# Kernel optimization log

Hardware: AMD Instinct MI355X
Metric: run time of the kernel (lower is better)

The kernel has to match this reference:

```python
import jax, jax.numpy as jnp
import numpy as np

NUM_HEADS = 12
HEAD_DIM = 64
HIDDEN = NUM_HEADS * HEAD_DIM  # 768
B, L = 4, 512

def setup_inputs() -> dict:
    key = jax.random.key(0)
    ks = jax.random.split(key, 8)
    s = 0.02
    return {
        "hidden_states": jax.random.normal(ks[0], (B, L, HIDDEN), jnp.float32),
        "relation_embedding_k": jax.random.normal(ks[1], (B, L, L, HEAD_DIM), jnp.float32),
        "relation_embedding_v": jax.random.normal(ks[2], (B, L, L, HEAD_DIM), jnp.float32),
        "Wq": jax.random.normal(ks[3], (HIDDEN, HIDDEN), jnp.float32) * s,
        "bq": jnp.zeros((HIDDEN,), jnp.float32),
        "Wk": jax.random.normal(ks[4], (HIDDEN, HIDDEN), jnp.float32) * s,
        "bk": jnp.zeros((HIDDEN,), jnp.float32),
        "Wv": jax.random.normal(ks[5], (HIDDEN, HIDDEN), jnp.float32) * s,
        "bv": jnp.zeros((HIDDEN,), jnp.float32),
    }

def _heads(x):
    # [B, L, HIDDEN] -> [B, H, L, D]
    b, l, _ = x.shape
    return x.reshape(b, l, NUM_HEADS, HEAD_DIM).transpose(0, 2, 1, 3)

def reference(hidden_states, relation_embedding_k, relation_embedding_v,
              Wq, bq, Wk, bk, Wv, bv):
    q = _heads(hidden_states @ Wq + bq)  # [B,H,L,D]
    k = _heads(hidden_states @ Wk + bk)
    v = _heads(hidden_states @ Wv + bv)

    # content scores + relation key scores (shared across heads)
    scores = jnp.einsum('bhld,bhmd->bhlm', q, k)
    scores = scores + jnp.einsum('bhld,blrd->bhlr', q, relation_embedding_k)
    scores = scores / np.sqrt(HEAD_DIM).astype(np.float32)

    probs = jax.nn.softmax(scores, axis=-1)  # [B,H,L,L]

    ctx = jnp.einsum('bhlm,bhmd->bhld', probs, v)
    ctx = ctx + jnp.einsum('bhlr,brld->bhld', probs, relation_embedding_v)

    # [B,H,L,D] -> [B,L,HIDDEN]
    b, h, l, d = ctx.shape
    return ctx.transpose(0, 2, 1, 3).reshape(b, l, h * d)
```

## Files before the change

kernel.cpp:

```cpp
#include <hip/hip_runtime.h>
#include <stdint.h>


typedef __attribute__((ext_vector_type(8))) short bf16x8;
typedef __attribute__((ext_vector_type(4))) float f32x4;
typedef __attribute__((ext_vector_type(4))) unsigned int u32x4;
typedef __attribute__((ext_vector_type(2))) unsigned int u32x2;

__device__ __forceinline__ unsigned short f2bf(float f) {
  union { float f; unsigned int u; } v; v.f = f;
  unsigned int r = v.u + 0x7fffu + ((v.u >> 16) & 1u);
  return (unsigned short)(r >> 16);
}
__device__ __forceinline__ float bf2f(unsigned short s) {
  union { unsigned int u; float f; } v; v.u = ((unsigned int)s) << 16;
  return v.f;
}
__device__ __forceinline__ void lds_barrier() {
  asm volatile("s_waitcnt lgkmcnt(0)\ns_barrier" ::: "memory");
}

__global__ void k_cvt_hidden(const float* __restrict__ x, unsigned short* __restrict__ y) {
  int i = blockIdx.x * 256 + threadIdx.x;
  float4 v = reinterpret_cast<const float4*>(x)[i];
  ushort4 o;
  o.x = f2bf(v.x); o.y = f2bf(v.y); o.z = f2bf(v.z); o.w = f2bf(v.w);
  reinterpret_cast<ushort4*>(y)[i] = o;
}

__global__ void k_transp_w(const float* __restrict__ Wq, const float* __restrict__ Wk,
                           const float* __restrict__ Wv, unsigned short* __restrict__ wt) {
  __shared__ float t[64][65];
  const int kt = blockIdx.x, nt = blockIdx.y, wsel = blockIdx.z;
  const float* W = wsel == 0 ? Wq : (wsel == 1 ? Wk : Wv);
  const int lx = threadIdx.x & 63, ly = threadIdx.x >> 6;
  for (int i = 0; i < 64; i += 4)
    t[ly + i][lx] = W[(size_t)(kt * 64 + ly + i) * 768 + nt * 64 + lx];
  __syncthreads();
  for (int i = 0; i < 64; i += 4) {
    int r = ly + i;
    wt[((size_t)wsel * 768 + nt * 64 + r) * 768 + kt * 64 + lx] = f2bf(t[lx][r]);
  }
}

__global__ __launch_bounds__(256) void k_qkv_gemm(
    const unsigned short* __restrict__ A, const unsigned short* __restrict__ Bt,
    const float* __restrict__ bq, const float* __restrict__ bk, const float* __restrict__ bv,
    unsigned short* __restrict__ qbf, unsigned short* __restrict__ kbf,
    unsigned short* __restrict__ vbt) {
  __shared__ __align__(16) unsigned short lA[64 * 64];
  __shared__ __align__(16) unsigned short lB[64 * 64];
  const int tid = threadIdx.x, lane = tid & 63, w = tid >> 6;
  const int m0 = blockIdx.x * 64, n0 = blockIdx.y * 64;
  const int wm = (w >> 1) * 32, wn = (w & 1) * 32;
  f32x4 acc[2][2] = {};

  for (int kt = 0; kt < 12; ++kt) {
    __syncthreads();
#pragma unroll
    for (int i = 0; i < 2; ++i) {
      int e16 = i * 256 + tid;
      int row = e16 >> 3;
      int kb = (e16 & 7) * 16;
      int dst = row * 128 + (kb ^ ((row & 7) << 4));
      u32x4 va = *(const u32x4*)((const char*)A + (size_t)(m0 + row) * 1536 + kt * 128 + kb);
      *(u32x4*)((char*)lA + dst) = va;
      u32x4 vb = *(const u32x4*)((const char*)Bt + (size_t)(n0 + row) * 1536 + kt * 128 + kb);
      *(u32x4*)((char*)lB + dst) = vb;
    }
    __syncthreads();
#pragma unroll
    for (int ks = 0; ks < 2; ++ks) {
      bf16x8 fa[2], fb[2];
      const int kbyte = (ks * 32 + (lane >> 4) * 8) * 2;
#pragma unroll
      for (int mi = 0; mi < 2; ++mi) {
        int row = wm + mi * 16 + (lane & 15);
        fa[mi] = *(const bf16x8*)((const char*)lA + row * 128 + (kbyte ^ ((row & 7) << 4)));
      }
#pragma unroll
      for (int ni = 0; ni < 2; ++ni) {
        int row = wn + ni * 16 + (lane & 15);
        fb[ni] = *(const bf16x8*)((const char*)lB + row * 128 + (kbyte ^ ((row & 7) << 4)));
      }
#pragma unroll
      for (int mi = 0; mi < 2; ++mi)
#pragma unroll
        for (int ni = 0; ni < 2; ++ni)
          acc[mi][ni] = __builtin_amdgcn_mfma_f32_16x16x32_bf16(fa[mi], fb[ni], acc[mi][ni], 0, 0, 0);
    }
  }
#pragma unroll
  for (int mi = 0; mi < 2; ++mi)
#pragma unroll
    for (int ni = 0; ni < 2; ++ni) {
      int gn = n0 + wn + ni * 16 + (lane & 15);
      float bias = (gn < 768) ? bq[gn] : (gn < 1536 ? bk[gn - 768] : bv[gn - 1536]);
#pragma unroll
      for (int r = 0; r < 4; ++r) {
        int gm = m0 + wm + mi * 16 + ((lane >> 4) << 2) + r;
        float val = acc[mi][ni][r] + bias;
        int b = gm >> 9, l = gm & 511;
        int d = gn & 63;
        if (gn < 768) {
          int h = gn >> 6;
          qbf[(((size_t)(b * 12 + h)) * 512 + l) * 64 + d] = f2bf(val);
        } else if (gn < 1536) {
          int h = (gn - 768) >> 6;
          kbf[(((size_t)(b * 12 + h)) * 512 + l) * 64 + d] = f2bf(val);
        } else {
          int h = (gn - 1536) >> 6;
          vbt[(((size_t)(b * 12 + h)) * 64 + d) * 512 + l] = f2bf(val);
        }
      }
    }
}

__global__ __launch_bounds__(256) void k_scores(
    const unsigned short* __restrict__ qbf, const unsigned short* __restrict__ kbf,
    float* __restrict__ S) {
  __shared__ __align__(16) unsigned short lQ[64 * 64];
  __shared__ __align__(16) unsigned short lK[64 * 64];
  const int tid = threadIdx.x, lane = tid & 63, w = tid >> 6;
  const int mt = blockIdx.x, lt = blockIdx.y, bh = blockIdx.z;
  const int wm = (w >> 1) * 32, wn = (w & 1) * 32;
  f32x4 acc[2][2] = {};
#pragma unroll
  for (int i = 0; i < 2; ++i) {
    int e16 = i * 256 + tid;
    int row = e16 >> 3;
    int kb = (e16 & 7) * 16;
    int dst = row * 128 + (kb ^ ((row & 7) << 4));
    u32x4 vq = *(const u32x4*)((const char*)qbf + ((size_t)bh * 512 + lt * 64 + row) * 128 + kb);
    *(u32x4*)((char*)lQ + dst) = vq;
    u32x4 vk = *(const u32x4*)((const char*)kbf + ((size_t)bh * 512 + mt * 64 + row) * 128 + kb);
    *(u32x4*)((char*)lK + dst) = vk;
  }
  __syncthreads();
#pragma unroll
  for (int ks = 0; ks < 2; ++ks) {
    bf16x8 fa[2], fb[2];
    const int kbyte = (ks * 32 + (lane >> 4) * 8) * 2;
#pragma unroll
    for (int mi = 0; mi < 2; ++mi) {
      int row = wm + mi * 16 + (lane & 15);
      fa[mi] = *(const bf16x8*)((const char*)lQ + row * 128 + (kbyte ^ ((row & 7) << 4)));
    }
#pragma unroll
    for (int ni = 0; ni < 2; ++ni) {
      int row = wn + ni * 16 + (lane & 15);
      fb[ni] = *(const bf16x8*)((const char*)lK + row * 128 + (kbyte ^ ((row & 7) << 4)));
    }
#pragma unroll
    for (int mi = 0; mi < 2; ++mi)
#pragma unroll
      for (int ni = 0; ni < 2; ++ni)
        acc[mi][ni] = __builtin_amdgcn_mfma_f32_16x16x32_bf16(fa[mi], fb[ni], acc[mi][ni], 0, 0, 0);
  }
#pragma unroll
  for (int mi = 0; mi < 2; ++mi)
#pragma unroll
    for (int ni = 0; ni < 2; ++ni) {
      int gm = mt * 64 + wn + ni * 16 + (lane & 15);
#pragma unroll
      for (int r = 0; r < 4; ++r) {
        int gl = lt * 64 + wm + mi * 16 + ((lane >> 4) << 2) + r;
        S[(size_t)bh * 262144 + (size_t)gl * 512 + gm] = acc[mi][ni][r];
      }
    }
}

__global__ __launch_bounds__(256, 3) void k_rel(
    const unsigned short* __restrict__ qbf,
    const float* __restrict__ relk,
    const float* __restrict__ relv,
    const float* __restrict__ S,
    unsigned short* __restrict__ pbf,
    float* __restrict__ crel) {
  __shared__ __align__(16) char X[32768];
  __shared__ __align__(16) unsigned short ps[16 * 512];
  const int tid = threadIdx.x, lane = tid & 63, w = tid >> 6;
  const int bl = blockIdx.x, b = bl >> 9, l = bl & 511;
  const int lm = lane & 15, lg = lane >> 4;
  const int rr = tid >> 4, xc = tid & 15;

  {
    u32x4 zz = {0u, 0u, 0u, 0u};
    *(u32x4*)((char*)ps + 12288 + tid * 16) = zz;
  }

  const int hq = lm < 12 ? lm : 11;
  const char* qrow = (const char*)qbf + (((size_t)b * 12 + hq) * 512 + l) * 128;
  const bf16x8 qa0 = *(const bf16x8*)(qrow + lg * 16);
  const bf16x8 qa1 = *(const bf16x8*)(qrow + 64 + lg * 16);

  const char* rkbase = (const char*)relk + (size_t)bl * 131072;
  const char* rvbase = (const char*)relv + (size_t)b * 67108864 + (size_t)l * 256;

  f32x4 stg[2][8];
  f32x4 accA[4][2];
#pragma unroll
  for (int t = 0; t < 4; ++t) {
    accA[t][0] = {0.f, 0.f, 0.f, 0.f};
    accA[t][1] = {0.f, 0.f, 0.f, 0.f};
  }

#pragma unroll
  for (int i = 0; i < 8; ++i)
    stg[0][i] = *(const f32x4*)(rkbase + (size_t)(i * 16 + rr) * 256 + xc * 16);

#pragma unroll
  for (int t = 0; t < 4; ++t) {
    if (t < 3) {
#pragma unroll
      for (int i = 0; i < 8; ++i)
        stg[(t + 1) & 1][i] =
            *(const f32x4*)(rkbase + (size_t)((t + 1) * 128 + i * 16 + rr) * 256 + xc * 16);
    }
    char* buf = X + (t & 1) * 16384;
#pragma unroll
    for (int i = 0; i < 8; ++i) {
      const int rl = i * 16 + rr;
      f32x4 v = stg[t & 1][i];
      u32x2 pk;
      pk.x = (unsigned)f2bf(v[0]) | ((unsigned)f2bf(v[1]) << 16);
      pk.y = (unsigned)f2bf(v[2]) | ((unsigned)f2bf(v[3]) << 16);
      *(u32x2*)(buf + rl * 128 + ((xc * 8) ^ ((rl & 7) << 4))) = pk;
    }
    lds_barrier();
#pragma unroll
    for (int p = 0; p < 2; ++p) {
      const int rrow = (w * 2 + p) * 16 + lm;
      const char* base = buf + rrow * 128;
      bf16x8 fb0 = *(const bf16x8*)(base + ((lg * 16) ^ ((rrow & 7) << 4)));
      bf16x8 fb1 = *(const bf16x8*)(base + ((64 + lg * 16) ^ ((rrow & 7) << 4)));
      accA[t][p] = __builtin_amdgcn_mfma_f32_16x16x32_bf16(qa0, fb0, accA[t][p], 0, 0, 0);
      accA[t][p] = __builtin_amdgcn_mfma_f32_16x16x32_bf16(qa1, fb1, accA[t][p], 0, 0, 0);
    }
  }

  float sreg[3][8];
#pragma unroll
  for (int hh = 0; hh < 3; ++hh) {
    const float* sp = S + (((size_t)b * 12 + (w * 3 + hh)) * 512 + l) * 512 + lane;
#pragma unroll
    for (int j = 0; j < 8; ++j) sreg[hh][j] = sp[j * 64];
  }

  lds_barrier();
  if (lg < 3) {
#pragma unroll
    for (int t = 0; t < 4; ++t)
#pragma unroll
      for (int p = 0; p < 2; ++p) {
        const int r = t * 128 + w * 32 + p * 16 + lm;
#pragma unroll
        for (int reg = 0; reg < 4; ++reg) {
          const int h = lg * 4 + reg;
          *(float*)(X + h * 2048 + ((r * 4) ^ ((h & 7) << 4))) = accA[t][p][reg];
        }
      }
  }
  lds_barrier();

#pragma unroll
  for (int i = 0; i < 8; ++i)
    stg[0][i] = *(const f32x4*)(rvbase + (size_t)(i * 16 + rr) * 131072 + xc * 16);

#pragma unroll
  for (int hh = 0; hh < 3; ++hh) {
    const int h = w * 3 + hh;
    const size_t srow = (((size_t)b * 12 + h) * 512 + l) * 512;
    float sv[8];
    float mx = -1e30f;
#pragma unroll
    for (int j = 0; j < 8; ++j) {
      const int r = j * 64 + lane;
      float sr = *(const float*)(X + h * 2048 + ((r * 4) ^ ((h & 7) << 4)));
      float s = (sr + sreg[hh][j]) * 0.125f;
      sv[j] = s;
      mx = fmaxf(mx, s);
    }
#pragma unroll
    for (int off = 32; off; off >>= 1) mx = fmaxf(mx, __shfl_xor(mx, off));
    float sm = 0.f;
#pragma unroll
    for (int j = 0; j < 8; ++j) { sv[j] = __expf(sv[j] - mx); sm += sv[j]; }
#pragma unroll
    for (int off = 32; off; off >>= 1) sm += __shfl_xor(sm, off);
    const float inv = 1.f / sm;
#pragma unroll
    for (int j = 0; j < 8; ++j) {
      const int r = j * 64 + lane;
      const unsigned short pb = f2bf(sv[j] * inv);
      *(unsigned short*)((char*)ps + h * 1024 + ((r * 2) ^ ((h & 7) << 4))) = pb;
      pbf[srow + r] = pb;
    }
  }
  lds_barrier();

  f32x4 accC = {0.f, 0.f, 0.f, 0.f};
#pragma unroll
  for (int t = 0; t < 4; ++t) {
    if (t < 3) {
#pragma unroll
      for (int i = 0; i < 8; ++i)
        stg[(t + 1) & 1][i] =
            *(const f32x4*)(rvbase + (size_t)((t + 1) * 128 + i * 16 + rr) * 131072 + xc * 16);
    }
    char* buf = X + (t & 1) * 16384;
#pragma unroll
    for (int i = 0; i < 8; ++i) {
      const int rl = i * 16 + rr;
      f32x4 v = stg[t & 1][i];
#pragma unroll
      for (int e = 0; e < 4; ++e) {
        const int d = xc * 4 + e;
        *(unsigned short*)(buf + d * 256 + ((rl * 2) ^ ((d & 15) << 4))) = f2bf(v[e]);
      }
    }
    lds_barrier();
    const int drow = w * 16 + lm;
    const char* abase = buf + drow * 256;
#pragma unroll
    for (int kk = 0; kk < 4; ++kk) {
      bf16x8 fa = *(const bf16x8*)(abase + (((kk * 32 + lg * 8) * 2) ^ ((drow & 15) << 4)));
      const int rg = t * 128 + kk * 32 + lg * 8;
      bf16x8 fp = *(const bf16x8*)((const char*)ps + lm * 1024 + ((rg * 2) ^ ((lm & 7) << 4)));
      accC = __builtin_amdgcn_mfma_f32_16x16x32_bf16(fa, fp, accC, 0, 0, 0);
    }
  }
  if (lm < 12) {
#pragma unroll
    for (int reg = 0; reg < 4; ++reg)
      crel[(size_t)bl * 768 + lm * 64 + w * 16 + lg * 4 + reg] = accC[reg];
  }
}

__global__ __launch_bounds__(256) void k_pv(
    const unsigned short* __restrict__ pbf, const unsigned short* __restrict__ vbt,
    const float* __restrict__ crel, float* __restrict__ out) {
  __shared__ __align__(16) unsigned short lP[64 * 64];
  __shared__ __align__(16) unsigned short lV[64 * 64];
  const int tid = threadIdx.x, lane = tid & 63, w = tid >> 6;
  const int lt = blockIdx.x, bh = blockIdx.y;
  const int b = bh / 12, h = bh % 12;
  const int wm = (w >> 1) * 32, wn = (w & 1) * 32;
  f32x4 acc[2][2] = {};
  const char* pbase = (const char*)pbf + ((size_t)bh * 512 + lt * 64) * 1024;
  const char* vbase = (const char*)vbt + (size_t)bh * 64 * 1024;
  for (int kt = 0; kt < 8; ++kt) {
    __syncthreads();
#pragma unroll
    for (int i = 0; i < 2; ++i) {
      int e16 = i * 256 + tid;
      int row = e16 >> 3;
      int kb = (e16 & 7) * 16;
      int dst = row * 128 + (kb ^ ((row & 7) << 4));
      u32x4 vp = *(const u32x4*)(pbase + (size_t)row * 1024 + kt * 128 + kb);
      *(u32x4*)((char*)lP + dst) = vp;
      u32x4 vv = *(const u32x4*)(vbase + (size_t)row * 1024 + kt * 128 + kb);
      *(u32x4*)((char*)lV + dst) = vv;
    }
    __syncthreads();
#pragma unroll
    for (int ks = 0; ks < 2; ++ks) {
      bf16x8 fa[2], fb[2];
      const int kbyte = (ks * 32 + (lane >> 4) * 8) * 2;
#pragma unroll
      for (int mi = 0; mi < 2; ++mi) {
        int row = wm + mi * 16 + (lane & 15);
        fa[mi] = *(const bf16x8*)((const char*)lP + row * 128 + (kbyte ^ ((row & 7) << 4)));
      }
#pragma unroll
      for (int ni = 0; ni < 2; ++ni) {
        int row = wn + ni * 16 + (lane & 15);
        fb[ni] = *(const bf16x8*)((const char*)lV + row * 128 + (kbyte ^ ((row & 7) << 4)));
      }
#pragma unroll
      for (int mi = 0; mi < 2; ++mi)
#pragma unroll
        for (int ni = 0; ni < 2; ++ni)
          acc[mi][ni] = __builtin_amdgcn_mfma_f32_16x16x32_bf16(fa[mi], fb[ni], acc[mi][ni], 0, 0, 0);
    }
  }
#pragma unroll
  for (int mi = 0; mi < 2; ++mi)
#pragma unroll
    for (int ni = 0; ni < 2; ++ni) {
      int gd = wn + ni * 16 + (lane & 15);
#pragma unroll
      for (int r = 0; r < 4; ++r) {
        int gl = lt * 64 + wm + mi * 16 + ((lane >> 4) << 2) + r;
        size_t o = ((size_t)b * 512 + gl) * 768 + h * 64 + gd;
        out[o] = acc[mi][ni][r] + crel[o];
      }
    }
}

extern "C" void kernel_launch(void* const* d_in, const int* in_sizes, int n_in,
                              void* d_out, int out_size, void* d_ws, size_t ws_size,
                              hipStream_t stream) {
  (void)in_sizes; (void)n_in; (void)out_size; (void)ws_size;
  const float* hidden = (const float*)d_in[0];
  const float* relk   = (const float*)d_in[1];
  const float* relv   = (const float*)d_in[2];
  const float* Wq     = (const float*)d_in[3];
  const float* bq     = (const float*)d_in[4];
  const float* Wk     = (const float*)d_in[5];
  const float* bk     = (const float*)d_in[6];
  const float* Wv     = (const float*)d_in[7];
  const float* bv     = (const float*)d_in[8];
  float* out = (float*)d_out;
  char* ws = (char*)d_ws;

  unsigned short* hb  = (unsigned short*)(ws);
  unsigned short* wt  = (unsigned short*)(ws + 3145728);
  unsigned short* qbf = (unsigned short*)(ws + 6684672);
  unsigned short* kbf = (unsigned short*)(ws + 9830400);
  unsigned short* vbt = (unsigned short*)(ws + 12976128);
  float*          S   = (float*)(ws + 16121856);
  unsigned short* pbf = (unsigned short*)(ws + 66453504);
  float*          cr  = (float*)(ws + 91619328);

  k_cvt_hidden<<<1536, 256, 0, stream>>>(hidden, hb);
  k_transp_w<<<dim3(12, 12, 3), 256, 0, stream>>>(Wq, Wk, Wv, wt);
  k_qkv_gemm<<<dim3(32, 36), 256, 0, stream>>>(hb, wt, bq, bk, bv, qbf, kbf, vbt);
  k_scores<<<dim3(8, 8, 48), 256, 0, stream>>>(qbf, kbf, S);
  k_rel<<<2048, 256, 0, stream>>>(qbf, relk, relv, S, pbf, cr);
  k_pv<<<dim3(8, 48), 256, 0, stream>>>(pbf, vbt, cr, out);
}
```

Baseline: 189.1 us.

## Load relation tensors directly into registers and compute relv context in fp32 FMA

The relation-key scores now load rel_k fp32 straight from global memory into MFMA fragment registers with a 3-deep register prefetch, skipping the LDS staging and barriers. The relation-value context drops the bf16 MFMA path. Each wave streams its own slice of rel_v rows with coalesced per-lane float loads, does fp32 FMAs against fp32 probabilities kept in LDS, and the four waves' partial sums are reduced through LDS. This cuts LDS traffic and the occupancy hint, and reduces the bf16 conversion of rel_v, at the cost of more scalar FMA work and narrower 4-byte loads.

```diff
diff --git a/kernel.cpp b/kernel.cpp
--- a/kernel.cpp
+++ b/kernel.cpp
@@ -5,7 +5,6 @@
 typedef __attribute__((ext_vector_type(8))) short bf16x8;
 typedef __attribute__((ext_vector_type(4))) float f32x4;
 typedef __attribute__((ext_vector_type(4))) unsigned int u32x4;
-typedef __attribute__((ext_vector_type(2))) unsigned int u32x2;
 
 __device__ __forceinline__ unsigned short f2bf(float f) {
   union { float f; unsigned int u; } v; v.f = f;
@@ -170,74 +169,56 @@
     }
 }
 
-__global__ __launch_bounds__(256, 3) void k_rel(
+__global__ __launch_bounds__(256) void k_rel(
     const unsigned short* __restrict__ qbf,
     const float* __restrict__ relk,
     const float* __restrict__ relv,
     const float* __restrict__ S,
     unsigned short* __restrict__ pbf,
     float* __restrict__ crel) {
-  __shared__ __align__(16) char X[32768];
-  __shared__ __align__(16) unsigned short ps[16 * 512];
+  __shared__ __align__(16) char X[24576];
   const int tid = threadIdx.x, lane = tid & 63, w = tid >> 6;
   const int bl = blockIdx.x, b = bl >> 9, l = bl & 511;
   const int lm = lane & 15, lg = lane >> 4;
-  const int rr = tid >> 4, xc = tid & 15;
-
-  {
-    u32x4 zz = {0u, 0u, 0u, 0u};
-    *(u32x4*)((char*)ps + 12288 + tid * 16) = zz;
-  }
 
   const int hq = lm < 12 ? lm : 11;
   const char* qrow = (const char*)qbf + (((size_t)b * 12 + hq) * 512 + l) * 128;
   const bf16x8 qa0 = *(const bf16x8*)(qrow + lg * 16);
   const bf16x8 qa1 = *(const bf16x8*)(qrow + 64 + lg * 16);
 
-  const char* rkbase = (const char*)relk + (size_t)bl * 131072;
-  const char* rvbase = (const char*)relv + (size_t)b * 67108864 + (size_t)l * 256;
-
-  f32x4 stg[2][8];
-  f32x4 accA[4][2];
-#pragma unroll
-  for (int t = 0; t < 4; ++t) {
-    accA[t][0] = {0.f, 0.f, 0.f, 0.f};
-    accA[t][1] = {0.f, 0.f, 0.f, 0.f};
-  }
-
-#pragma unroll
-  for (int i = 0; i < 8; ++i)
-    stg[0][i] = *(const f32x4*)(rkbase + (size_t)(i * 16 + rr) * 256 + xc * 16);
-
-#pragma unroll
-  for (int t = 0; t < 4; ++t) {
-    if (t < 3) {
-#pragma unroll
-      for (int i = 0; i < 8; ++i)
-        stg[(t + 1) & 1][i] =
-            *(const f32x4*)(rkbase + (size_t)((t + 1) * 128 + i * 16 + rr) * 256 + xc * 16);
-    }
-    char* buf = X + (t & 1) * 16384;
-#pragma unroll
-    for (int i = 0; i < 8; ++i) {
-      const int rl = i * 16 + rr;
-      f32x4 v = stg[t & 1][i];
-      u32x2 pk;
-      pk.x = (unsigned)f2bf(v[0]) | ((unsigned)f2bf(v[1]) << 16);
-      pk.y = (unsigned)f2bf(v[2]) | ((unsigned)f2bf(v[3]) << 16);
-      *(u32x2*)(buf + rl * 128 + ((xc * 8) ^ ((rl & 7) << 4))) = pk;
-    }
-    lds_barrier();
-#pragma unroll
-    for (int p = 0; p < 2; ++p) {
-      const int rrow = (w * 2 + p) * 16 + lm;
-      const char* base = buf + rrow * 128;
-      bf16x8 fb0 = *(const bf16x8*)(base + ((lg * 16) ^ ((rrow & 7) << 4)));
-      bf16x8 fb1 = *(const bf16x8*)(base + ((64 + lg * 16) ^ ((rrow & 7) << 4)));
-      accA[t][p] = __builtin_amdgcn_mfma_f32_16x16x32_bf16(qa0, fb0, accA[t][p], 0, 0, 0);
-      accA[t][p] = __builtin_amdgcn_mfma_f32_16x16x32_bf16(qa1, fb1, accA[t][p], 0, 0, 0);
-    }
-  }
+  const char* rkb = (const char*)relk + (size_t)bl * 131072 +
+                    (size_t)(w * 128 + lm) * 256 + lg * 32;
+  f32x4 ld[3][4];
+  f32x4 accA[8];
+#pragma unroll
+  for (int t = 0; t < 8; ++t) accA[t] = {0.f, 0.f, 0.f, 0.f};
+
+#define LOADT(t, s)                                                  \
+  {                                                                  \
+    const char* p_ = rkb + (size_t)(t) * 4096;                       \
+    ld[s][0] = *(const f32x4*)(p_);                                  \
+    ld[s][1] = *(const f32x4*)(p_ + 16);                             \
+    ld[s][2] = *(const f32x4*)(p_ + 128);                            \
+    ld[s][3] = *(const f32x4*)(p_ + 144);                            \
+  }
+  LOADT(0, 0)
+  LOADT(1, 1)
+#pragma unroll
+  for (int t = 0; t < 8; ++t) {
+    if (t < 6) LOADT(t + 2, (t + 2) % 3)
+    union { bf16x8 v; unsigned short u[8]; } fb0, fb1;
+    const int s = t % 3;
+#pragma unroll
+    for (int j = 0; j < 4; ++j) {
+      fb0.u[j] = f2bf(ld[s][0][j]);
+      fb0.u[4 + j] = f2bf(ld[s][1][j]);
+      fb1.u[j] = f2bf(ld[s][2][j]);
+      fb1.u[4 + j] = f2bf(ld[s][3][j]);
+    }
+    accA[t] = __builtin_amdgcn_mfma_f32_16x16x32_bf16(qa0, fb0.v, accA[t], 0, 0, 0);
+    accA[t] = __builtin_amdgcn_mfma_f32_16x16x32_bf16(qa1, fb1.v, accA[t], 0, 0, 0);
+  }
+#undef LOADT
 
   float sreg[3][8];
 #pragma unroll
@@ -247,37 +228,30 @@
     for (int j = 0; j < 8; ++j) sreg[hh][j] = sp[j * 64];
   }
 
+  if (lg < 3) {
+#pragma unroll
+    for (int t = 0; t < 8; ++t) {
+      const int r = w * 128 + t * 16 + lm;
+#pragma unroll
+      for (int reg = 0; reg < 4; ++reg) {
+        const int h = lg * 4 + reg;
+        *(float*)(X + h * 2048 + ((r * 4) ^ (lg << 6))) = accA[t][reg];
+      }
+    }
+  }
   lds_barrier();
-  if (lg < 3) {
-#pragma unroll
-    for (int t = 0; t < 4; ++t)
-#pragma unroll
-      for (int p = 0; p < 2; ++p) {
-        const int r = t * 128 + w * 32 + p * 16 + lm;
-#pragma unroll
-        for (int reg = 0; reg < 4; ++reg) {
-          const int h = lg * 4 + reg;
-          *(float*)(X + h * 2048 + ((r * 4) ^ ((h & 7) << 4))) = accA[t][p][reg];
-        }
-      }
-  }
-  lds_barrier();
-
-#pragma unroll
-  for (int i = 0; i < 8; ++i)
-    stg[0][i] = *(const f32x4*)(rvbase + (size_t)(i * 16 + rr) * 131072 + xc * 16);
 
 #pragma unroll
   for (int hh = 0; hh < 3; ++hh) {
     const int h = w * 3 + hh;
+    const int sw = ((h >> 2) & 3) << 6;
     const size_t srow = (((size_t)b * 12 + h) * 512 + l) * 512;
     float sv[8];
     float mx = -1e30f;
 #pragma unroll
     for (int j = 0; j < 8; ++j) {
       const int r = j * 64 + lane;
-      float sr = *(const float*)(X + h * 2048 + ((r * 4) ^ ((h & 7) << 4)));
-      float s = (sr + sreg[hh][j]) * 0.125f;
+      float s = (*(const float*)(X + h * 2048 + ((r * 4) ^ sw)) + sreg[hh][j]) * 0.125f;
       sv[j] = s;
       mx = fmaxf(mx, s);
     }
@@ -292,48 +266,41 @@
 #pragma unroll
     for (int j = 0; j < 8; ++j) {
       const int r = j * 64 + lane;
-      const unsigned short pb = f2bf(sv[j] * inv);
-      *(unsigned short*)((char*)ps + h * 1024 + ((r * 2) ^ ((h & 7) << 4))) = pb;
-      pbf[srow + r] = pb;
+      const float pv = sv[j] * inv;
+      *(float*)(X + h * 2048 + ((r * 4) ^ sw)) = pv;
+      pbf[srow + r] = f2bf(pv);
     }
   }
   lds_barrier();
 
-  f32x4 accC = {0.f, 0.f, 0.f, 0.f};
-#pragma unroll
-  for (int t = 0; t < 4; ++t) {
-    if (t < 3) {
-#pragma unroll
-      for (int i = 0; i < 8; ++i)
-        stg[(t + 1) & 1][i] =
-            *(const f32x4*)(rvbase + (size_t)((t + 1) * 128 + i * 16 + rr) * 131072 + xc * 16);
-    }
-    char* buf = X + (t & 1) * 16384;
-#pragma unroll
-    for (int i = 0; i < 8; ++i) {
-      const int rl = i * 16 + rr;
-      f32x4 v = stg[t & 1][i];
-#pragma unroll
-      for (int e = 0; e < 4; ++e) {
-        const int d = xc * 4 + e;
-        *(unsigned short*)(buf + d * 256 + ((rl * 2) ^ ((d & 15) << 4))) = f2bf(v[e]);
-      }
-    }
-    lds_barrier();
-    const int drow = w * 16 + lm;
-    const char* abase = buf + drow * 256;
-#pragma unroll
-    for (int kk = 0; kk < 4; ++kk) {
-      bf16x8 fa = *(const bf16x8*)(abase + (((kk * 32 + lg * 8) * 2) ^ ((drow & 15) << 4)));
-      const int rg = t * 128 + kk * 32 + lg * 8;
-      bf16x8 fp = *(const bf16x8*)((const char*)ps + lm * 1024 + ((rg * 2) ^ ((lm & 7) << 4)));
-      accC = __builtin_amdgcn_mfma_f32_16x16x32_bf16(fa, fp, accC, 0, 0, 0);
-    }
-  }
-  if (lm < 12) {
-#pragma unroll
-    for (int reg = 0; reg < 4; ++reg)
-      crel[(size_t)bl * 768 + lm * 64 + w * 16 + lg * 4 + reg] = accC[reg];
+  float cacc[12];
+#pragma unroll
+  for (int h = 0; h < 12; ++h) cacc[h] = 0.f;
+  const char* vptr = (const char*)relv + (size_t)b * 67108864 +
+                     (size_t)(w * 128) * 131072 + (size_t)l * 256 + lane * 4;
+#pragma unroll 2
+  for (int rc = 0; rc < 32; ++rc) {
+    const float v0 = *(const float*)(vptr);
+    const float v1 = *(const float*)(vptr + 131072);
+    const float v2 = *(const float*)(vptr + 262144);
+    const float v3 = *(const float*)(vptr + 393216);
+    vptr += 524288;
+    const int r0 = w * 128 + rc * 4;
+#pragma unroll
+    for (int h = 0; h < 12; ++h) {
+      const f32x4 p = *(const f32x4*)(X + h * 2048 + ((r0 * 4) ^ (((h >> 2) & 3) << 6)));
+      cacc[h] += p[0] * v0 + p[1] * v1 + p[2] * v2 + p[3] * v3;
+    }
+  }
+  lds_barrier();
+  float* red = (float*)X;
+#pragma unroll
+  for (int h = 0; h < 12; ++h) red[(w * 12 + h) * 64 + lane] = cacc[h];
+  lds_barrier();
+  for (int i = tid; i < 768; i += 256) {
+    const int h = i >> 6, d = i & 63;
+    crel[(size_t)bl * 768 + i] =
+        red[h * 64 + d] + red[(12 + h) * 64 + d] + red[(24 + h) * 64 + d] + red[(36 + h) * 64 + d];
   }
 }
 
```

New measurement: 198.8 us. 1.05x slower.
